# Kernel tuning notes

Measured on AMD Instinct MI355X. Metric: run time of the kernel, lower is better.

Reference implementation:

```python
import jax, jax.numpy as jnp
import numpy as np

N = 100000       # nodes
E = 1600000      # edges
F_IN = 128       # num_features
DIM = 128        # hidden dim
L = 3            # num_gc_layers
G = 512          # num graphs
EPS = 1e-5       # BatchNorm eps


def setup_inputs() -> dict:
    key = jax.random.key(0)
    ks = jax.random.split(key, 3 + 4 * L)
    d = {
        "x": jax.random.normal(ks[0], (N, F_IN), jnp.float32),
        "edge_index": jax.random.randint(ks[1], (2, E), 0, N, dtype=jnp.int32).astype(jnp.int64),
        "batch": jnp.sort(jax.random.randint(ks[2], (N,), 0, G, dtype=jnp.int32)).astype(jnp.int64),
    }
    fin = F_IN
    for i in range(L):
        d[f"W{i}"] = jax.random.normal(ks[3 + 4 * i], (fin, DIM), jnp.float32) / np.float32(np.sqrt(fin))
        d[f"b{i}"] = jnp.zeros((DIM,), jnp.float32)
        d[f"g{i}"] = jnp.ones((DIM,), jnp.float32)   # BN gamma
        d[f"t{i}"] = jnp.zeros((DIM,), jnp.float32)  # BN beta
        fin = DIM
    return d


def _gcn_layer(h, src, dst, norm, W, b):
    # GCNConv: (xW) gathered at src, degree-normalized, scatter-added at dst, + bias
    h = h @ W                                    # [N, DIM] small GEMM
    msg = h[src] * norm[:, None]                 # [E+N, DIM] gather (memory-bound)
    out = jax.ops.segment_sum(msg, dst, num_segments=N)
    return out + b


def _forward(x, edge_index, batch, params):
    loops = jnp.arange(N, dtype=edge_index.dtype)
    src = jnp.concatenate([edge_index[0], loops])   # add self-loops (PyG default)
    dst = jnp.concatenate([edge_index[1], loops])
    deg = jax.ops.segment_sum(jnp.ones_like(src, jnp.float32), dst, num_segments=N)
    dinv = jax.lax.rsqrt(jnp.maximum(deg, 1.0))     # deg >= 1 due to self-loops
    norm = dinv[src] * dinv[dst]

    pools = []
    h = x
    for (W, b, g, t) in params:
        h = jax.nn.relu(_gcn_layer(h, src, dst, norm, W, b))
        # BatchNorm1d (training-mode batch stats, biased variance)
        mu = h.mean(axis=0)
        var = h.var(axis=0)
        h = (h - mu) * jax.lax.rsqrt(var + EPS) * g + t
        # global_add_pool per layer
        pools.append(jax.ops.segment_sum(h, batch, num_segments=G))
    return jnp.concatenate(pools, axis=1)  # [G, L*DIM]


def reference(x, edge_index, batch, W0, b0, g0, t0, W1, b1, g1, t1, W2, b2, g2, t2):
    params = [(W0, b0, g0, t0), (W1, b1, g1, t1), (W2, b2, g2, t2)]
    return _forward(x, edge_index, batch, params)
```

## Files before the change

kernel.cpp:

```cpp
#include <hip/hip_runtime.h>

#define NNODES 100000
#define NEDGES 1600000
#define NGRAPH 512
#define EPSBN 1e-5f
#define DEGCAP 64
#define NBUCK 256
#define BSH 9
#define BCAP 9216
#define P1_BLOCKS ((NEDGES + 4095)/4096)
#define GEMM_BLOCKS ((NNODES + 63)/64)

typedef unsigned short ushort_t;
typedef unsigned int uint_t;

typedef __attribute__((ext_vector_type(8))) __bf16 bf16x8;
typedef __attribute__((ext_vector_type(4))) float f32x4;
typedef __attribute__((ext_vector_type(2))) uint_t uintx2;

__device__ __forceinline__ float b2f(ushort_t u){ return __uint_as_float(((uint_t)u)<<16); }
__device__ __forceinline__ ushort_t f2b(float f){
  uint_t x = __float_as_uint(f);
  uint_t r = (x + 0x7fffu + ((x>>16)&1u))>>16;
  return (ushort_t)r;
}
__device__ __forceinline__ float lo16(uint_t d){ return b2f((ushort_t)(d & 0xffffu)); }
__device__ __forceinline__ float hi16(uint_t d){ return b2f((ushort_t)(d >> 16)); }

__device__ __forceinline__ f32x4 mfma_bf16(bf16x8 a, bf16x8 b, f32x4 c){
  return __builtin_amdgcn_mfma_f32_16x16x32_bf16(a, b, c, 0, 0, 0);
}

union Frag8 { ushort_t u[8]; bf16x8 v; };

__device__ __forceinline__ bf16x8 cvt8_f32_bf16(const float* __restrict__ p){
  float4 v0 = *(const float4*)(const void*)p;
  float4 v1 = *(const float4*)(const void*)(p + 4);
  Frag8 f;
  f.u[0] = f2b(v0.x); f.u[1] = f2b(v0.y); f.u[2] = f2b(v0.z); f.u[3] = f2b(v0.w);
  f.u[4] = f2b(v1.x); f.u[5] = f2b(v1.y); f.u[6] = f2b(v1.z); f.u[7] = f2b(v1.w);
  return f.v;
}

__global__ __launch_bounds__(256) void k_p1(const int* __restrict__ src,
                                            const int* __restrict__ dst,
                                            int* __restrict__ gBucket,
                                            int2* __restrict__ ebuf,
                                            const int* __restrict__ batch,
                                            int* __restrict__ gstart,
                                            const float* __restrict__ x,
                                            const float* __restrict__ W0,
                                            ushort_t* __restrict__ hs){
  __shared__ __attribute__((aligned(16))) ushort_t sMem[128*136];

  if (blockIdx.x < P1_BLOCKS){
    int* cntL  = (int*)sMem;
    int* baseL = cntL + NBUCK;
    int* ofsL  = baseL + NBUCK;
    int t = threadIdx.x;
    if (t < NBUCK){ cntL[t] = 0; ofsL[t] = 0; }
    __syncthreads();

    int base = blockIdx.x * 4096;
    int e0 = base + t*16;
    int s[16], d[16];
    int ne = 0;
    if (e0 + 16 <= NEDGES){
      #pragma unroll
      for (int q = 0; q < 4; ++q){
        int4 sv = *(const int4*)(src + e0 + q*4);
        int4 dv = *(const int4*)(dst + e0 + q*4);
        s[q*4+0]=sv.x; s[q*4+1]=sv.y; s[q*4+2]=sv.z; s[q*4+3]=sv.w;
        d[q*4+0]=dv.x; d[q*4+1]=dv.y; d[q*4+2]=dv.z; d[q*4+3]=dv.w;
      }
      ne = 16;
    } else {
      for (int e = e0; e < NEDGES && ne < 16; ++e, ++ne){
        s[ne] = src[e]; d[ne] = dst[e];
      }
    }
    for (int k = 0; k < ne; ++k) atomicAdd(&cntL[d[k] >> BSH], 1);
    __syncthreads();
    if (t < NBUCK){
      int c = cntL[t];
      baseL[t] = c ? atomicAdd(&gBucket[t*16], c) : 0;
    }
    __syncthreads();
    for (int k = 0; k < ne; ++k){
      int b = d[k] >> BSH;
      int o = atomicAdd(&ofsL[b], 1);
      ebuf[(size_t)b*BCAP + baseL[b] + o] = make_int2(s[k], d[k]);
    }
    return;
  }
  if (blockIdx.x == P1_BLOCKS){
    #pragma unroll
    for (int r = 0; r < 2; ++r){
      int g = threadIdx.x + r*256;
      int lo = 0, hi = NNODES;
      while (lo < hi){
        int mid = (lo + hi) >> 1;
        if (batch[mid] < g) lo = mid + 1; else hi = mid;
      }
      gstart[g] = lo;
    }
    if (threadIdx.x == 0) gstart[NGRAPH] = NNODES;
    return;
  }

  ushort_t* sWT = sMem;
  int bb = blockIdx.x - P1_BLOCKS - 1;
  for (int idx = threadIdx.x; idx < 128*128; idx += 256){
    int c = idx >> 7, jj = idx & 127;
    sWT[jj*136 + c] = f2b(W0[idx]);
  }
  __syncthreads();

  int wave = threadIdx.x >> 6;
  int lane = threadIdx.x & 63;
  int quad = lane >> 4;
  int l16  = lane & 15;
  int row0 = bb*64 + wave*16;

  int m  = row0 + l16;
  int mc = (m < NNODES) ? m : (NNODES - 1);

  const float* ap = x + (size_t)mc*128 + quad*8;
  bf16x8 af0 = cvt8_f32_bf16(ap);
  bf16x8 af1 = cvt8_f32_bf16(ap + 32);
  bf16x8 af2 = cvt8_f32_bf16(ap + 64);
  bf16x8 af3 = cvt8_f32_bf16(ap + 96);

  f32x4 acc[8];
  #pragma unroll
  for (int ct = 0; ct < 8; ++ct){
    const ushort_t* bp = sWT + (ct*16 + l16)*136 + quad*8;
    bf16x8 b0 = *(const bf16x8*)(const void*)(bp);
    bf16x8 b1 = *(const bf16x8*)(const void*)(bp + 32);
    bf16x8 b2 = *(const bf16x8*)(const void*)(bp + 64);
    bf16x8 b3 = *(const bf16x8*)(const void*)(bp + 96);
    f32x4 a_ = {0.f, 0.f, 0.f, 0.f};
    a_ = mfma_bf16(af0, b0, a_);
    a_ = mfma_bf16(af1, b1, a_);
    a_ = mfma_bf16(af2, b2, a_);
    a_ = mfma_bf16(af3, b3, a_);
    acc[ct] = a_;
  }

  int rbase = row0 + quad*4;
  #pragma unroll
  for (int ct = 0; ct < 8; ++ct){
    int colc = ct*16 + l16;
    #pragma unroll
    for (int rg = 0; rg < 4; ++rg){
      int rr = rbase + rg;
      if (rr < NNODES) hs[(size_t)rr*128 + colc] = f2b(acc[ct][rg]);
    }
  }
}

__global__ __launch_bounds__(256) void k_p2(const int2* __restrict__ ebuf,
                                            const int* __restrict__ gBucket,
                                            int* __restrict__ colx,
                                            int* __restrict__ cnt,
                                            ushort_t* __restrict__ hs){
  __shared__ int slotcnt[512];
  int t = threadIdx.x;
  int b = blockIdx.x;
  slotcnt[t] = 0; slotcnt[t + 256] = 0;
  __syncthreads();

  int nb = gBucket[b*16];
  int vbase = b << BSH;

  for (int e = t; e < nb; e += 256){
    int2 p = ebuf[(size_t)b*BCAP + e];
    int slot = atomicAdd(&slotcnt[p.y - vbase], 1);
    colx[p.y*DEGCAP + slot] = p.x;
  }
  __syncthreads();

  #pragma unroll
  for (int r = 0; r < 2; ++r){
    int i = t + r*256;
    int v = vbase + i;
    if (v < NNODES){
      int c = slotcnt[i];
      cnt[v] = c;
      int ce = (c <= 15) ? 15 : 31;
      for (int s = c; s < ce; ++s) colx[(size_t)v*DEGCAP + s] = NNODES;
    }
  }

  uint_t* H = (uint_t*)hs;
  for (int idx = t; idx < 512*64; idx += 256){
    int r = idx >> 6;
    int v = vbase + r;
    if (v < NNODES){
      int lane = idx & 63;
      float dv = rsqrtf((float)(slotcnt[r] + 1));
      uint_t d = H[(uint_t)v*64u + lane];
      H[(uint_t)v*64u + lane] = (uint_t)f2b(lo16(d)*dv) | ((uint_t)f2b(hi16(d)*dv) << 16);
    }
  }
}

__global__ __launch_bounds__(256) void k_gemm(const ushort_t* __restrict__ A,
                                              const ushort_t* __restrict__ WT,
                                              const float* __restrict__ Kv,
                                              const int* __restrict__ cnt,
                                              ushort_t* __restrict__ hs){
  __shared__ __attribute__((aligned(16))) ushort_t sWT[128*136];
  {
    const uint4* sp = (const uint4*)WT;
    uint4* dp = (uint4*)sWT;
    for (int i = threadIdx.x; i < (128*136*2)/16; i += 256) dp[i] = sp[i];
  }
  __syncthreads();

  int wave = threadIdx.x >> 6;
  int lane = threadIdx.x & 63;
  int quad = lane >> 4;
  int l16  = lane & 15;
  int row0 = blockIdx.x*64 + wave*16;

  int m  = row0 + l16;
  int mc = (m < NNODES) ? m : (NNODES - 1);

  const ushort_t* ap = A + (size_t)mc*128 + quad*8;
  bf16x8 af0 = *(const bf16x8*)(const void*)(ap);
  bf16x8 af1 = *(const bf16x8*)(const void*)(ap + 32);
  bf16x8 af2 = *(const bf16x8*)(const void*)(ap + 64);
  bf16x8 af3 = *(const bf16x8*)(const void*)(ap + 96);

  f32x4 acc[8];
  #pragma unroll
  for (int ct = 0; ct < 8; ++ct){
    const ushort_t* bp = sWT + (ct*16 + l16)*136 + quad*8;
    bf16x8 b0 = *(const bf16x8*)(const void*)(bp);
    bf16x8 b1 = *(const bf16x8*)(const void*)(bp + 32);
    bf16x8 b2 = *(const bf16x8*)(const void*)(bp + 64);
    bf16x8 b3 = *(const bf16x8*)(const void*)(bp + 96);
    f32x4 a_ = {0.f, 0.f, 0.f, 0.f};
    a_ = mfma_bf16(af0, b0, a_);
    a_ = mfma_bf16(af1, b1, a_);
    a_ = mfma_bf16(af2, b2, a_);
    a_ = mfma_bf16(af3, b3, a_);
    acc[ct] = a_;
  }

  int rbase = row0 + quad*4;
  float dv[4];
  #pragma unroll
  for (int rg = 0; rg < 4; ++rg){
    int rr = rbase + rg;
    int cc = cnt[(rr < NNODES) ? rr : (NNODES - 1)];
    dv[rg] = rsqrtf((float)(cc + 1));
  }
  #pragma unroll
  for (int ct = 0; ct < 8; ++ct){
    int colc = ct*16 + l16;
    float kv = Kv[colc];
    #pragma unroll
    for (int rg = 0; rg < 4; ++rg){
      int rr = rbase + rg;
      if (rr < NNODES){
        float val = (acc[ct][rg] + kv) * dv[rg];
        hs[(size_t)rr*128 + colc] = f2b(val);
      }
    }
  }
}

#define AGG_BLOCKS 1024
#define AGG_WAVES (AGG_BLOCKS*4)
#define AGG_CHUNK ((NNODES + AGG_WAVES - 1) / AGG_WAVES)

#define FENCE8(A) asm volatile("" :: \
  "v"(A[0]),"v"(A[1]),"v"(A[2]),"v"(A[3]),"v"(A[4]),"v"(A[5]),"v"(A[6]),"v"(A[7]))

#define ISSUE_R0(dst, cr, vv) do { \
  _Pragma("unroll") \
  for (int k_ = 0; k_ < 8; ++k_){ \
    int uA_ = (k_ == 0) ? (vv) : __builtin_amdgcn_readlane((cr), 2*k_ - 1); \
    int uB_ = __builtin_amdgcn_readlane((cr), 2*k_); \
    int u_  = sel ? uB_ : uA_; \
    (dst)[k_] = H2[(uint_t)u_*32u + m]; \
  } \
} while(0)

#define ISSUE_R1(dst, cr) do { \
  _Pragma("unroll") \
  for (int k_ = 0; k_ < 8; ++k_){ \
    int uA_ = __builtin_amdgcn_readlane((cr), 15 + 2*k_); \
    int uB_ = __builtin_amdgcn_readlane((cr), 16 + 2*k_); \
    int u_  = sel ? uB_ : uA_; \
    (dst)[k_] = H2[(uint_t)u_*32u + m]; \
  } \
} while(0)

#define CONSUME8(A) do { \
  FENCE8(A); \
  _Pragma("unroll") \
  for (int k_ = 0; k_ < 8; ++k_){ \
    a0 += lo16((A)[k_].x); a1 += hi16((A)[k_].x); \
    a2 += lo16((A)[k_].y); a3 += hi16((A)[k_].y); \
  } \
} while(0)

template<bool WR>
__global__ __launch_bounds__(256, 4) void k_agg(const ushort_t* __restrict__ hs,
                                                const int* __restrict__ cnt,
                                                const int* __restrict__ colx,
                                                const float* __restrict__ bias,
                                                const int* __restrict__ batch,
                                                ushort_t* __restrict__ rout,
                                                float* __restrict__ poolS,
                                                float* __restrict__ chansum,
                                                float* __restrict__ chansumsq){
  __shared__ float bsum[128];
  __shared__ float bsq[128];
  if (threadIdx.x < 128){ bsum[threadIdx.x] = 0.f; bsq[threadIdx.x] = 0.f; }
  __syncthreads();

  int wave = __builtin_amdgcn_readfirstlane((blockIdx.x << 2) + (threadIdx.x >> 6));
  int lane = threadIdx.x & 63;
  int m    = lane & 31;
  int sel  = lane >> 5;
  int n0 = wave * AGG_CHUNK;
  int n1 = (n0 + AGG_CHUNK < NNODES) ? (n0 + AGG_CHUNK) : NNODES;

  const uintx2* H2 = (const uintx2*)hs;
  uintx2* R2 = (uintx2*)rout;

  float bbv[4];
  #pragma unroll
  for (int i = 0; i < 4; ++i) bbv[i] = bias[4*m + i];
  int chbase = 4*m + 2*sel;

  float ss0 = 0.f, ss1 = 0.f, sq0 = 0.f, sq1 = 0.f;
  float p0 = 0.f, p1 = 0.f;
  int curg = -1;

  if (n0 < n1){
    int cr0 = colx[(size_t)n0*DEGCAP + lane];
    int cv0 = cnt[n0];
    int cr1 = 0, cv1 = 0;
    if (n0 + 1 < n1){
      cr1 = colx[(size_t)(n0+1)*DEGCAP + lane];
      cv1 = cnt[n0+1];
    }
    uintx2 e0[8], e1[8];
    ISSUE_R0(e0, cr0, n0);
    if (cv0 > 15) ISSUE_R1(e1, cr0);
    else { _Pragma("unroll") for (int k_ = 0; k_ < 8; ++k_) e1[k_] = (uintx2){0u,0u}; }

    for (int v = n0; v < n1; ++v){
      int v2 = v + 2;
      int cr2 = 0, cv2 = 0;
      if (v2 < n1){
        cr2 = colx[(size_t)v2*DEGCAP + lane];
        cv2 = cnt[v2];
      }

      uintx2 f0[8], f1[8];
      bool hasn = (v + 1 < n1);
      if (hasn){
        ISSUE_R0(f0, cr1, v + 1);
        if (cv1 > 15) ISSUE_R1(f1, cr1);
        else { _Pragma("unroll") for (int k_ = 0; k_ < 8; ++k_) f1[k_] = (uintx2){0u,0u}; }
      } else {
        _Pragma("unroll") for (int k_ = 0; k_ < 8; ++k_){ f0[k_] = (uintx2){0u,0u}; f1[k_] = (uintx2){0u,0u}; }
      }

      int g = batch[v];
      if (g != curg){
        if (curg >= 0){
          atomicAdd(&poolS[curg*128 + chbase],     p0);
          atomicAdd(&poolS[curg*128 + chbase + 1], p1);
        }
        p0 = 0.f; p1 = 0.f; curg = g;
      }

      float a0 = 0.f, a1 = 0.f, a2 = 0.f, a3 = 0.f;

      CONSUME8(e0);
      if (cv0 > 15) CONSUME8(e1);
      if (cv0 > 31){
        for (int j = 31; j < cv0; j += 2){
          int uA = __builtin_amdgcn_readlane(cr0, j);
          int uB = (j + 1 < cv0) ? __builtin_amdgcn_readlane(cr0, j + 1) : NNODES;
          int u  = sel ? uB : uA;
          uintx2 dd = H2[(uint_t)u*32u + m];
          a0 += lo16(dd.x); a1 += hi16(dd.x);
          a2 += lo16(dd.y); a3 += hi16(dd.y);
        }
      }

      float s0 = a0 + __shfl_xor(a0, 32, 64);
      float s1 = a1 + __shfl_xor(a1, 32, 64);
      float s2 = a2 + __shfl_xor(a2, 32, 64);
      float s3 = a3 + __shfl_xor(a3, 32, 64);

      float dvv = rsqrtf((float)(cv0 + 1));
      float r0 = fmaxf(s0*dvv + bbv[0], 0.f);
      float r1 = fmaxf(s1*dvv + bbv[1], 0.f);
      float r2 = fmaxf(s2*dvv + bbv[2], 0.f);
      float r3 = fmaxf(s3*dvv + bbv[3], 0.f);
      if constexpr (WR){
        if (lane < 32){
          uintx2 wv;
          wv.x = (uint_t)f2b(r0) | ((uint_t)f2b(r1) << 16);
          wv.y = (uint_t)f2b(r2) | ((uint_t)f2b(r3) << 16);
          R2[(uint_t)v*32u + m] = wv;
        }
      }
      float cA = sel ? r2 : r0;
      float cB = sel ? r3 : r1;
      ss0 += cA; ss1 += cB;
      sq0 += cA*cA; sq1 += cB*cB;
      p0 += cA; p1 += cB;

      cr0 = cr1; cv0 = cv1;
      cr1 = cr2; cv1 = cv2;
      #pragma unroll
      for (int k_ = 0; k_ < 8; ++k_){ e0[k_] = f0[k_]; e1[k_] = f1[k_]; }
    }
  }

  if (curg >= 0){
    atomicAdd(&poolS[curg*128 + chbase],     p0);
    atomicAdd(&poolS[curg*128 + chbase + 1], p1);
  }
  atomicAdd(&bsum[chbase],     ss0);
  atomicAdd(&bsum[chbase + 1], ss1);
  atomicAdd(&bsq[chbase],      sq0);
  atomicAdd(&bsq[chbase + 1],  sq1);
  __syncthreads();
  if (threadIdx.x < 128){
    atomicAdd(&chansum[threadIdx.x],   bsum[threadIdx.x]);
    atomicAdd(&chansumsq[threadIdx.x], bsq[threadIdx.x]);
  }
}

__global__ void k_fold(const float* __restrict__ Wn,
                       const float* __restrict__ chansum, const float* __restrict__ chansumsq,
                       const float* __restrict__ gamma, const float* __restrict__ beta,
                       ushort_t* __restrict__ WT, float* __restrict__ Kv,
                       float* __restrict__ avec, float* __restrict__ cvec){
  __shared__ float red[128];
  int j = blockIdx.x, c = threadIdx.x;
  const float invN = 1.0f / (float)NNODES;
  float mu  = chansum[c] * invN;
  float var = chansumsq[c] * invN - mu*mu;
  float a = gamma[c] * rsqrtf(var + EPSBN);
  float cc = beta[c] - mu*a;
  if (j == 0){ avec[c] = a; cvec[c] = cc; }
  float wv = Wn[c*128 + j];
  WT[j*136 + c] = f2b(a * wv);
  red[c] = cc * wv;
  __syncthreads();
  for (int off = 64; off > 0; off >>= 1){
    if (c < off) red[c] += red[c + off];
    __syncthreads();
  }
  if (c == 0) Kv[j] = red[0];
}

__global__ void k_final(const float* __restrict__ poolS, const int* __restrict__ gstart,
                        const float* __restrict__ avec, const float* __restrict__ cvec,
                        const float* __restrict__ chansum2, const float* __restrict__ chansumsq2,
                        const float* __restrict__ gamma2, const float* __restrict__ beta2,
                        float* __restrict__ out){
  int g = blockIdx.x, c = threadIdx.x;
  float n = (float)(gstart[g + 1] - gstart[g]);
  #pragma unroll
  for (int i = 0; i < 2; ++i){
    float v = avec[i*128 + c] * poolS[((size_t)i*NGRAPH + g)*128 + c] + n * cvec[i*128 + c];
    out[(size_t)g*384 + i*128 + c] = v;
  }
  const float invN = 1.0f / (float)NNODES;
  float mu  = chansum2[c] * invN;
  float var = chansumsq2[c] * invN - mu*mu;
  float a2 = gamma2[c] * rsqrtf(var + EPSBN);
  float c2 = beta2[c] - mu*a2;
  float v2 = a2 * poolS[((size_t)2*NGRAPH + g)*128 + c] + n * c2;
  out[(size_t)g*384 + 2*128 + c] = v2;
}

extern "C" void kernel_launch(void* const* d_in, const int* in_sizes, int n_in,
                              void* d_out, int out_size, void* d_ws, size_t ws_size,
                              hipStream_t stream){
  (void)in_sizes; (void)n_in; (void)out_size; (void)ws_size;

  const float* x     = (const float*)d_in[0];
  const int*   ei    = (const int*)d_in[1];
  const int*   batch = (const int*)d_in[2];
  const float* Wp[3] = {(const float*)d_in[3], (const float*)d_in[7],  (const float*)d_in[11]};
  const float* bp[3] = {(const float*)d_in[4], (const float*)d_in[8],  (const float*)d_in[12]};
  const float* gp[3] = {(const float*)d_in[5], (const float*)d_in[9],  (const float*)d_in[13]};
  const float* tp[3] = {(const float*)d_in[6], (const float*)d_in[10], (const float*)d_in[14]};
  const int* srcp = ei;
  const int* dstp = ei + NEDGES;

  char* w = (char*)d_ws;
  size_t off = 0;
  auto take = [&](size_t bytes) -> char* {
    char* p = w + off;
    off += (bytes + 511) & ~(size_t)511;
    return p;
  };
  int*      cnt       = (int*)take((size_t)NNODES*4);
  int*      colx      = (int*)take((size_t)NNODES*DEGCAP*4);
  int*      gstart    = (int*)take((NGRAPH+1)*4);
  ushort_t* hs        = (ushort_t*)take((size_t)(NNODES+1)*128*2);
  ushort_t* rbuf      = (ushort_t*)take((size_t)NNODES*128*2);
  ushort_t* WT        = (ushort_t*)take(128*136*2);
  float*    Kv        = (float*)take(128*4);
  float*    chanstats = (float*)take(3*256*4);
  float*    poolS     = (float*)take((size_t)3*NGRAPH*128*4);
  float*    avec      = (float*)take(2*128*4);
  float*    cvec      = (float*)take(2*128*4);
  int*      gBucket   = (int*)take(NBUCK*16*4);

  int2* ebuf = (int2*)rbuf;

  hipMemsetAsync(gBucket,   0, NBUCK*16*4,             stream);
  hipMemsetAsync(poolS,     0, (size_t)3*NGRAPH*128*4, stream);
  hipMemsetAsync(chanstats, 0, 3*256*4,                stream);
  hipMemsetAsync(hs + (size_t)NNODES*128, 0, 128*2,    stream);

  k_p1<<<P1_BLOCKS + 1 + GEMM_BLOCKS, 256, 0, stream>>>(
      srcp, dstp, gBucket, ebuf, batch, gstart, x, Wp[0], hs);
  k_p2<<<NBUCK, 256, 0, stream>>>(ebuf, gBucket, colx, cnt, hs);

  k_agg<true><<<AGG_BLOCKS, 256, 0, stream>>>(hs, cnt, colx, bp[0], batch, rbuf,
                                              poolS, chanstats, chanstats + 128);
  k_fold<<<128, 128, 0, stream>>>(Wp[1], chanstats, chanstats + 128,
                                  gp[0], tp[0], WT, Kv, avec, cvec);
  k_gemm<<<GEMM_BLOCKS, 256, 0, stream>>>(rbuf, WT, Kv, cnt, hs);
  k_agg<true><<<AGG_BLOCKS, 256, 0, stream>>>(hs, cnt, colx, bp[1], batch, rbuf,
                                              poolS + (size_t)NGRAPH*128,
                                              chanstats + 256, chanstats + 256 + 128);
  k_fold<<<128, 128, 0, stream>>>(Wp[2], chanstats + 256, chanstats + 256 + 128,
                                  gp[1], tp[1], WT, Kv, avec + 128, cvec + 128);
  k_gemm<<<GEMM_BLOCKS, 256, 0, stream>>>(rbuf, WT, Kv, cnt, hs);
  k_agg<false><<<AGG_BLOCKS, 256, 0, stream>>>(hs, cnt, colx, bp[2], batch, rbuf,
                                               poolS + (size_t)2*NGRAPH*128,
                                               chanstats + 512, chanstats + 512 + 128);

  k_final<<<NGRAPH, 128, 0, stream>>>(poolS, gstart, avec, cvec,
                                      chanstats + 512, chanstats + 512 + 128,
                                      gp[2], tp[2], (float*)d_out);
}
```

Before: 478.1 us.

## Use finer edge buckets and split source-row degree scaling into its own kernel

```diff
diff --git a/kernel.cpp b/kernel.cpp
--- a/kernel.cpp
+++ b/kernel.cpp
@@ -5,9 +5,9 @@
 #define NGRAPH 512
 #define EPSBN 1e-5f
 #define DEGCAP 64
-#define NBUCK 256
-#define BSH 9
-#define BCAP 9216
+#define NBUCK 512
+#define BSH 8
+#define BCAP 4864
 #define P1_BLOCKS ((NEDGES + 4095)/4096)
 #define GEMM_BLOCKS ((NNODES + 63)/64)
 
@@ -20,9 +20,14 @@
 
 __device__ __forceinline__ float b2f(ushort_t u){ return __uint_as_float(((uint_t)u)<<16); }
 __device__ __forceinline__ ushort_t f2b(float f){
-  uint_t x = __float_as_uint(f);
-  uint_t r = (x + 0x7fffu + ((x>>16)&1u))>>16;
-  return (ushort_t)r;
+  union { __bf16 h; ushort_t u; } c;
+  c.h = (__bf16)f;
+  return c.u;
+}
+__device__ __forceinline__ uint_t pkbf(float a, float b){
+  union { __bf16 h[2]; uint_t u; } c;
+  c.h[0] = (__bf16)a; c.h[1] = (__bf16)b;
+  return c.u;
 }
 __device__ __forceinline__ float lo16(uint_t d){ return b2f((ushort_t)(d & 0xffffu)); }
 __device__ __forceinline__ float hi16(uint_t d){ return b2f((ushort_t)(d >> 16)); }
@@ -58,7 +63,11 @@
     int* baseL = cntL + NBUCK;
     int* ofsL  = baseL + NBUCK;
     int t = threadIdx.x;
-    if (t < NBUCK){ cntL[t] = 0; ofsL[t] = 0; }
+    #pragma unroll
+    for (int r = 0; r < 2; ++r){
+      int i = t + r*256;
+      cntL[i] = 0; ofsL[i] = 0;
+    }
     __syncthreads();
 
     int base = blockIdx.x * 4096;
@@ -81,9 +90,11 @@
     }
     for (int k = 0; k < ne; ++k) atomicAdd(&cntL[d[k] >> BSH], 1);
     __syncthreads();
-    if (t < NBUCK){
-      int c = cntL[t];
-      baseL[t] = c ? atomicAdd(&gBucket[t*16], c) : 0;
+    #pragma unroll
+    for (int r = 0; r < 2; ++r){
+      int i = t + r*256;
+      int c = cntL[i];
+      baseL[i] = c ? atomicAdd(&gBucket[i*16], c) : 0;
     }
     __syncthreads();
     for (int k = 0; k < ne; ++k){
@@ -162,12 +173,11 @@
 __global__ __launch_bounds__(256) void k_p2(const int2* __restrict__ ebuf,
                                             const int* __restrict__ gBucket,
                                             int* __restrict__ colx,
-                                            int* __restrict__ cnt,
-                                            ushort_t* __restrict__ hs){
-  __shared__ int slotcnt[512];
+                                            int* __restrict__ cnt){
+  __shared__ int slotcnt[256];
   int t = threadIdx.x;
   int b = blockIdx.x;
-  slotcnt[t] = 0; slotcnt[t + 256] = 0;
+  slotcnt[t] = 0;
   __syncthreads();
 
   int nb = gBucket[b*16];
@@ -180,28 +190,27 @@
   }
   __syncthreads();
 
-  #pragma unroll
-  for (int r = 0; r < 2; ++r){
-    int i = t + r*256;
-    int v = vbase + i;
-    if (v < NNODES){
-      int c = slotcnt[i];
-      cnt[v] = c;
-      int ce = (c <= 15) ? 15 : 31;
-      for (int s = c; s < ce; ++s) colx[(size_t)v*DEGCAP + s] = NNODES;
-    }
-  }
-
-  uint_t* H = (uint_t*)hs;
-  for (int idx = t; idx < 512*64; idx += 256){
-    int r = idx >> 6;
-    int v = vbase + r;
-    if (v < NNODES){
-      int lane = idx & 63;
-      float dv = rsqrtf((float)(slotcnt[r] + 1));
-      uint_t d = H[(uint_t)v*64u + lane];
-      H[(uint_t)v*64u + lane] = (uint_t)f2b(lo16(d)*dv) | ((uint_t)f2b(hi16(d)*dv) << 16);
-    }
+  int v = vbase + t;
+  if (v < NNODES){
+    int c = slotcnt[t];
+    cnt[v] = c;
+    int ce = (c <= 15) ? 15 : 31;
+    for (int s = c; s < ce; ++s) colx[(size_t)v*DEGCAP + s] = NNODES;
+  }
+}
+
+#define NORM_BLOCKS 1024
+__global__ __launch_bounds__(256) void k_norm(const int* __restrict__ cnt,
+                                              ushort_t* __restrict__ hs){
+  uintx2* H2 = (uintx2*)hs;
+  const int total = NNODES*32;
+  for (int i = blockIdx.x*256 + threadIdx.x; i < total; i += NORM_BLOCKS*256){
+    int v = i >> 5;
+    float dv = rsqrtf((float)(cnt[v] + 1));
+    uintx2 d = H2[i];
+    d.x = pkbf(lo16(d.x)*dv, hi16(d.x)*dv);
+    d.y = pkbf(lo16(d.y)*dv, hi16(d.y)*dv);
+    H2[i] = d;
   }
 }
 
@@ -410,8 +419,8 @@
       if constexpr (WR){
         if (lane < 32){
           uintx2 wv;
-          wv.x = (uint_t)f2b(r0) | ((uint_t)f2b(r1) << 16);
-          wv.y = (uint_t)f2b(r2) | ((uint_t)f2b(r3) << 16);
+          wv.x = pkbf(r0, r1);
+          wv.y = pkbf(r2, r3);
           R2[(uint_t)v*32u + m] = wv;
         }
       }
@@ -532,7 +541,8 @@
 
   k_p1<<<P1_BLOCKS + 1 + GEMM_BLOCKS, 256, 0, stream>>>(
       srcp, dstp, gBucket, ebuf, batch, gstart, x, Wp[0], hs);
-  k_p2<<<NBUCK, 256, 0, stream>>>(ebuf, gBucket, colx, cnt, hs);
+  k_p2<<<NBUCK, 256, 0, stream>>>(ebuf, gBucket, colx, cnt);
+  k_norm<<<NORM_BLOCKS, 256, 0, stream>>>(cnt, hs);
 
   k_agg<true><<<AGG_BLOCKS, 256, 0, stream>>>(hs, cnt, colx, bp[0], batch, rbuf,
                                               poolS, chanstats, chanstats + 128);
```

Result: faster. 442.8 us (-7.4%).
